# Kernel optimization log

Measured on AMD Instinct MI355X. Metric: run time of the kernel, lower is better.

## Reference

```python
import jax, jax.numpy as jnp
import numpy as np


def _window_indices(L, K):
    # 0-based (emo, cau) index pairs kept in the torch flattening order:
    # emo varies slowly (outer), cau varies fast (inner), |cau-emo| <= K.
    i = np.repeat(np.arange(L), L)
    j = np.tile(np.arange(L), L)
    m = np.abs(j - i) <= K
    return i[m], j[m]


def setup_inputs() -> dict:
    key = jax.random.key(0)
    ks = jax.random.split(key, 6)
    B, L, D = 4, 512, 768
    K, P = 10, 50
    R = 2 * D + P  # rank_feat_dim = 1586
    return {
        "doc_sents_h": jax.random.normal(ks[0], (B, L, D), jnp.float32),
        "pos_emb": jax.random.normal(ks[1], (2 * K + 1, P), jnp.float32) * 0.05,
        "W1": jax.random.normal(ks[2], (R, R), jnp.float32) * (1.0 / np.sqrt(R)),
        "b1": jax.random.normal(ks[3], (R,), jnp.float32) * 0.01,
        "W2": jax.random.normal(ks[4], (R, 1), jnp.float32) * (1.0 / np.sqrt(R)),
        "b2": jax.random.normal(ks[5], (1,), jnp.float32) * 0.01,
    }


def reference(doc_sents_h, pos_emb, W1, b1, W2, b2):
    B, L, D = doc_sents_h.shape
    K = (pos_emb.shape[0] - 1) // 2
    ei, ci = _window_indices(L, K)           # static numpy, shape [n]
    rel = jnp.asarray(ci - ei)               # [n] in [-K, K]
    # windowed pair features, [B, n, 2D] (skips the O(L^2) materialization)
    P_pairs = jnp.concatenate([doc_sents_h[:, ei], doc_sents_h[:, ci]], axis=-1)
    emb = pos_emb[rel + K]                   # [n, pos_dim]
    relf = rel.astype(pos_emb.dtype)
    kernel = jnp.exp(-jnp.square(relf[:, None] - relf[None, :]))  # [n, n]
    emb = kernel @ emb                       # [n, pos_dim], batch-invariant
    couples = jnp.concatenate(
        [P_pairs, jnp.broadcast_to(emb, (B,) + emb.shape)], axis=-1)  # [B, n, R]
    h = jax.nn.relu(couples @ W1 + b1)       # [B, n, R]
    pred = (h @ W2 + b2)[..., 0]             # [B, n]
    emo_cau_pos = jnp.stack(
        [jnp.asarray(ei) + 1, jnp.asarray(ci) + 1], axis=1)  # [n, 2], 1-based
    return pred, emo_cau_pos, h
```

## Files before the change

kernel.cpp:

```cpp
#include <hip/hip_runtime.h>
#include <math.h>

#define B_   4
#define L_   512
#define D_   768
#define K_   10
#define P_   50
#define R_   1586
#define NP_  10642
#define MROWS 2048
#define NPAD 1664
#define UVS  1600

#define PRED_OFF 0
#define POS_OFF  (B_ * NP_)
#define H_OFF    (B_ * NP_ + NP_ * 2)

typedef __attribute__((ext_vector_type(8))) short short8;
typedef __attribute__((ext_vector_type(4))) float floatx4;

__device__ __forceinline__ unsigned short f2bf(float f) {
    union { float f; unsigned int u; } a; a.f = f;
    unsigned int u = a.u;
    return (unsigned short)((u + 0x7FFF + ((u >> 16) & 1)) >> 16);
}
__device__ __forceinline__ float bf2f(unsigned short u) {
    union { unsigned int u; float f; } a; a.u = ((unsigned int)u) << 16;
    return a.f;
}

__device__ __forceinline__ int pair_offset(int i) {
    int h = i < K_ ? i : K_;
    int off = h * (K_ + 1) + (h * (h - 1)) / 2;
    if (i > K_) {
        int fullEnd = i < (L_ - K_) ? i : (L_ - K_);
        off += (fullEnd - K_) * (2 * K_ + 1);
        if (i > L_ - K_) {
            int t = i - (L_ - K_);
            int first = 2 * K_;
            int last = L_ + K_ - (i - 1);
            off += (first + last) * t / 2;
        }
    }
    return off;
}

__global__ __launch_bounds__(256) void convert_A(
        const float* __restrict__ doc, unsigned short* __restrict__ At) {
    int idx = (blockIdx.x * 256 + threadIdx.x) * 4;
    float4 v = *(const float4*)(doc + idx);
    ushort4 o;
    o.x = f2bf(v.x); o.y = f2bf(v.y); o.z = f2bf(v.z); o.w = f2bf(v.w);
    *(ushort4*)(At + idx) = o;
}

__global__ __launch_bounds__(256) void convert_W(
        const float* __restrict__ W1, unsigned short* __restrict__ Wt) {
    int z = blockIdx.z;
    int k0 = blockIdx.x * 32;
    int n0 = blockIdx.y * 32;
    __shared__ float tile[32][33];
    int tx = threadIdx.x & 31, ty = threadIdx.x >> 5;
    #pragma unroll
    for (int r = 0; r < 4; ++r) {
        int k = k0 + ty + r * 8;
        int n = n0 + tx;
        tile[ty + r * 8][tx] = (n < R_) ? W1[(size_t)(z * D_ + k) * R_ + n] : 0.f;
    }
    __syncthreads();
    #pragma unroll
    for (int r = 0; r < 4; ++r) {
        int n = n0 + ty + r * 8;
        int k = k0 + tx;
        Wt[(size_t)z * NPAD * D_ + (size_t)n * D_ + k] = f2bf(tile[tx][ty + r * 8]);
    }
}

__global__ __launch_bounds__(256) void build_F(
        const float* __restrict__ pos_emb, const float* __restrict__ W1,
        const float* __restrict__ b1, unsigned short* __restrict__ Fb) {
    int s = blockIdx.x;
    __shared__ float Es[P_];
    if (threadIdx.x < P_) {
        float acc = 0.f;
        #pragma unroll
        for (int r = 0; r <= 2 * K_; ++r) {
            float cnt = (float)(L_ - (r > K_ ? r - K_ : K_ - r));
            float d = (float)(s - r);
            acc += cnt * expf(-d * d) * pos_emb[r * P_ + threadIdx.x];
        }
        Es[threadIdx.x] = acc;
    }
    __syncthreads();
    for (int j = threadIdx.x; j < R_; j += blockDim.x) {
        float acc = b1[j];
        #pragma unroll 10
        for (int p = 0; p < P_; ++p)
            acc += Es[p] * W1[(2 * D_ + p) * R_ + j];
        Fb[s * UVS + j] = f2bf(acc);
    }
}

#define GLOAD_LDS16(g, l) __builtin_amdgcn_global_load_lds( \
    (const __attribute__((address_space(1))) void*)(g), \
    (__attribute__((address_space(3))) void*)(l), 16, 0, 0)

__global__ __launch_bounds__(256) void gemm_mfma(
        const unsigned short* __restrict__ At,
        const unsigned short* __restrict__ Wt,
        unsigned short* __restrict__ U, unsigned short* __restrict__ V) {
    __shared__ unsigned short Alds[128 * 32];
    __shared__ unsigned short Blds[128 * 32];
    const int tileN = blockIdx.x * 128;
    const int tileM = blockIdx.y * 128;
    const unsigned short* Bt = Wt + (size_t)blockIdx.z * NPAD * D_;
    unsigned short* C = blockIdx.z ? V : U;

    const int lane = threadIdx.x & 63;
    const int w = threadIdx.x >> 6;
    const int wm = (w & 1) * 64, wn = (w >> 1) * 64;
    const int quad = lane >> 4, l16 = lane & 15;

    floatx4 acc[4][4] = {};

    for (int k0 = 0; k0 < D_; k0 += 32) {
        #pragma unroll
        for (int t = 0; t < 2; ++t) {
            int g = (t * 4 + w) * 64 + lane;
            int m = g >> 2, c = g & 3;
            GLOAD_LDS16(At + (size_t)(tileM + m) * D_ + k0 + c * 8,
                        Alds + (t * 4 + w) * 512);
            GLOAD_LDS16(Bt + (size_t)(tileN + m) * D_ + k0 + c * 8,
                        Blds + (t * 4 + w) * 512);
        }
        __syncthreads();
        short8 a[4], b[4];
        #pragma unroll
        for (int im = 0; im < 4; ++im)
            a[im] = *(const short8*)&Alds[(wm + im * 16 + l16) * 32 + quad * 8];
        #pragma unroll
        for (int in = 0; in < 4; ++in)
            b[in] = *(const short8*)&Blds[(wn + in * 16 + l16) * 32 + quad * 8];
        #pragma unroll
        for (int im = 0; im < 4; ++im)
            #pragma unroll
            for (int in = 0; in < 4; ++in)
                acc[im][in] = __builtin_amdgcn_mfma_f32_16x16x32_bf16(
                    a[im], b[in], acc[im][in], 0, 0, 0);
        __syncthreads();
    }
    #pragma unroll
    for (int im = 0; im < 4; ++im) {
        #pragma unroll
        for (int in = 0; in < 4; ++in) {
            int col = tileN + wn + in * 16 + l16;
            if (col < R_) {
                #pragma unroll
                for (int r = 0; r < 4; ++r) {
                    int row = tileM + wm + im * 16 + quad * 4 + r;
                    C[(size_t)row * UVS + col] = f2bf(acc[im][in][r]);
                }
            }
        }
    }
}

#define NC2 13
__global__ __launch_bounds__(256) void epilogue(
        const unsigned short* __restrict__ U, const unsigned short* __restrict__ V,
        const unsigned short* __restrict__ Fb, const float* __restrict__ W2,
        const float* __restrict__ b2, float* __restrict__ out) {
    const int w    = threadIdx.x >> 6;
    const int lane = threadIdx.x & 63;
    const int i    = blockIdx.x * 4 + w;
    const int b    = blockIdx.y;
    const int half = blockIdx.z;

    const ushort2* u2  = (const ushort2*)(U + (size_t)(b * L_ + i) * UVS);
    const float2*  w2v = (const float2*)W2;

    float2 ur[NC2], wr[NC2];
    #pragma unroll
    for (int t = 0; t < NC2; ++t) {
        int c = lane + t * 64;
        if (c < R_ / 2) {
            ushort2 uu = u2[c];
            ur[t] = make_float2(bf2f(uu.x), bf2f(uu.y));
            wr[t] = w2v[c];
        }
    }

    const int base = i - K_ > 0 ? i - K_ : 0;
    const int poff = pair_offset(i);
    const float bias = b2[0];
    const int dj0 = half ? 11 : 0;
    const int dj1 = half ? 21 : 11;

    for (int dj = dj0; dj < dj1; ++dj) {
        int j = i - K_ + dj;
        if (j < 0 || j >= L_) continue;
        int p = poff + (j - base);
        const ushort2* v2 = (const ushort2*)(V + (size_t)(b * L_ + j) * UVS);
        const ushort2* f2 = (const ushort2*)(Fb + (size_t)dj * UVS);
        double* h2 = (double*)(out + H_OFF + (size_t)(b * NP_ + p) * R_);

        float acc = 0.f;
        #pragma unroll
        for (int t = 0; t < NC2; ++t) {
            int c = lane + t * 64;
            if (c < R_ / 2) {
                ushort2 vv = v2[c], ff = f2[c];
                float h0 = fmaxf(ur[t].x + bf2f(vv.x) + bf2f(ff.x), 0.f);
                float h1 = fmaxf(ur[t].y + bf2f(vv.y) + bf2f(ff.y), 0.f);
                union { float2 f; double d; } pk;
                pk.f = make_float2(h0, h1);
                __builtin_nontemporal_store(pk.d, h2 + c);
                acc += h0 * wr[t].x + h1 * wr[t].y;
            }
        }
        #pragma unroll
        for (int off = 32; off; off >>= 1) acc += __shfl_down(acc, off, 64);
        if (lane == 0) {
            out[PRED_OFF + b * NP_ + p] = acc + bias;
            if (b == 0) {
                out[POS_OFF + p * 2 + 0] = (float)(i + 1);
                out[POS_OFF + p * 2 + 1] = (float)(j + 1);
            }
        }
    }
}

extern "C" void kernel_launch(void* const* d_in, const int* in_sizes, int n_in,
                              void* d_out, int out_size, void* d_ws, size_t ws_size,
                              hipStream_t stream) {
    const float* doc     = (const float*)d_in[0];
    const float* pos_emb = (const float*)d_in[1];
    const float* W1      = (const float*)d_in[2];
    const float* b1      = (const float*)d_in[3];
    const float* W2      = (const float*)d_in[4];
    const float* b2      = (const float*)d_in[5];
    float* out = (float*)d_out;

    char* ws = (char*)d_ws;
    size_t off = 0;
    unsigned short* U  = (unsigned short*)(ws + off); off += (size_t)MROWS * UVS * 2;
    unsigned short* V  = (unsigned short*)(ws + off); off += (size_t)MROWS * UVS * 2;
    unsigned short* Fb = (unsigned short*)(ws + off); off += (size_t)21 * UVS * 2;
    off = (off + 255) & ~(size_t)255;
    unsigned short* At = (unsigned short*)(ws + off); off += (size_t)MROWS * D_ * 2;
    off = (off + 255) & ~(size_t)255;
    unsigned short* Wt = (unsigned short*)(ws + off);

    convert_A<<<MROWS * D_ / 1024, 256, 0, stream>>>(doc, At);
    convert_W<<<dim3(D_ / 32, NPAD / 32, 2), 256, 0, stream>>>(W1, Wt);
    build_F<<<21, 256, 0, stream>>>(pos_emb, W1, b1, Fb);
    gemm_mfma<<<dim3(NPAD / 128, MROWS / 128, 2), 256, 0, stream>>>(At, Wt, U, V);
    epilogue<<<dim3(L_ / 4, B_, 2), 256, 0, stream>>>(U, V, Fb, W2, b2, out);
}
```

Measured before the change: 372.7 us.

## Merge prep kernels into one launch and remap epilogue to one row per block

Combines the bf16 conversion of A, the transposed conversion of W1 and the positional-feature build into a single kernel, with block ranges choosing the task. This removes two launches and their gaps. The epilogue now gives each block one (batch, row) pair, and its four waves stride over the 21 window offsets. U and W2 are therefore loaded once per row rather than once per half. The catch is fewer, wider blocks with uneven wave work near the sequence edges, plus branch divergence across blocks inside the fused prep kernel.

```diff
diff --git a/kernel.cpp b/kernel.cpp
--- a/kernel.cpp
+++ b/kernel.cpp
@@ -45,42 +45,47 @@
     return off;
 }
 
-__global__ __launch_bounds__(256) void convert_A(
-        const float* __restrict__ doc, unsigned short* __restrict__ At) {
-    int idx = (blockIdx.x * 256 + threadIdx.x) * 4;
-    float4 v = *(const float4*)(doc + idx);
-    ushort4 o;
-    o.x = f2bf(v.x); o.y = f2bf(v.y); o.z = f2bf(v.z); o.w = f2bf(v.w);
-    *(ushort4*)(At + idx) = o;
-}
-
-__global__ __launch_bounds__(256) void convert_W(
-        const float* __restrict__ W1, unsigned short* __restrict__ Wt) {
-    int z = blockIdx.z;
-    int k0 = blockIdx.x * 32;
-    int n0 = blockIdx.y * 32;
+#define CA_BLOCKS 1536
+#define CW_BLOCKS 2496
+__global__ __launch_bounds__(256) void prep(
+        const float* __restrict__ doc, const float* __restrict__ pos_emb,
+        const float* __restrict__ W1, const float* __restrict__ b1,
+        unsigned short* __restrict__ At, unsigned short* __restrict__ Wt,
+        unsigned short* __restrict__ Fb) {
     __shared__ float tile[32][33];
-    int tx = threadIdx.x & 31, ty = threadIdx.x >> 5;
-    #pragma unroll
-    for (int r = 0; r < 4; ++r) {
-        int k = k0 + ty + r * 8;
-        int n = n0 + tx;
-        tile[ty + r * 8][tx] = (n < R_) ? W1[(size_t)(z * D_ + k) * R_ + n] : 0.f;
-    }
-    __syncthreads();
-    #pragma unroll
-    for (int r = 0; r < 4; ++r) {
-        int n = n0 + ty + r * 8;
-        int k = k0 + tx;
-        Wt[(size_t)z * NPAD * D_ + (size_t)n * D_ + k] = f2bf(tile[tx][ty + r * 8]);
-    }
-}
-
-__global__ __launch_bounds__(256) void build_F(
-        const float* __restrict__ pos_emb, const float* __restrict__ W1,
-        const float* __restrict__ b1, unsigned short* __restrict__ Fb) {
-    int s = blockIdx.x;
     __shared__ float Es[P_];
+    const int bid = blockIdx.x;
+
+    if (bid < CA_BLOCKS) {
+        int idx = (bid * 256 + threadIdx.x) * 4;
+        float4 v = *(const float4*)(doc + idx);
+        ushort4 o;
+        o.x = f2bf(v.x); o.y = f2bf(v.y); o.z = f2bf(v.z); o.w = f2bf(v.w);
+        *(ushort4*)(At + idx) = o;
+        return;
+    }
+    if (bid < CA_BLOCKS + CW_BLOCKS) {
+        int bb = bid - CA_BLOCKS;
+        int z = bb / 1248, rem = bb % 1248;
+        int k0 = (rem % 24) * 32;
+        int n0 = (rem / 24) * 32;
+        int tx = threadIdx.x & 31, ty = threadIdx.x >> 5;
+        #pragma unroll
+        for (int r = 0; r < 4; ++r) {
+            int k = k0 + ty + r * 8;
+            int n = n0 + tx;
+            tile[ty + r * 8][tx] = (n < R_) ? W1[(size_t)(z * D_ + k) * R_ + n] : 0.f;
+        }
+        __syncthreads();
+        #pragma unroll
+        for (int r = 0; r < 4; ++r) {
+            int n = n0 + ty + r * 8;
+            int k = k0 + tx;
+            Wt[(size_t)z * NPAD * D_ + (size_t)n * D_ + k] = f2bf(tile[tx][ty + r * 8]);
+        }
+        return;
+    }
+    int s = bid - (CA_BLOCKS + CW_BLOCKS);
     if (threadIdx.x < P_) {
         float acc = 0.f;
         #pragma unroll
@@ -92,7 +97,7 @@
         Es[threadIdx.x] = acc;
     }
     __syncthreads();
-    for (int j = threadIdx.x; j < R_; j += blockDim.x) {
+    for (int j = threadIdx.x; j < R_; j += 256) {
         float acc = b1[j];
         #pragma unroll 10
         for (int p = 0; p < P_; ++p)
@@ -172,9 +177,8 @@
         const float* __restrict__ b2, float* __restrict__ out) {
     const int w    = threadIdx.x >> 6;
     const int lane = threadIdx.x & 63;
-    const int i    = blockIdx.x * 4 + w;
-    const int b    = blockIdx.y;
-    const int half = blockIdx.z;
+    const int b    = blockIdx.x >> 9;
+    const int i    = blockIdx.x & (L_ - 1);
 
     const ushort2* u2  = (const ushort2*)(U + (size_t)(b * L_ + i) * UVS);
     const float2*  w2v = (const float2*)W2;
@@ -193,12 +197,10 @@
     const int base = i - K_ > 0 ? i - K_ : 0;
     const int poff = pair_offset(i);
     const float bias = b2[0];
-    const int dj0 = half ? 11 : 0;
-    const int dj1 = half ? 21 : 11;
-
-    for (int dj = dj0; dj < dj1; ++dj) {
+
+    for (int dj = w; dj < 2 * K_ + 1; dj += 4) {
         int j = i - K_ + dj;
-        if (j < 0 || j >= L_) continue;
+        if ((unsigned)j >= L_) continue;
         int p = poff + (j - base);
         const ushort2* v2 = (const ushort2*)(V + (size_t)(b * L_ + j) * UVS);
         const ushort2* f2 = (const ushort2*)(Fb + (size_t)dj * UVS);
@@ -251,9 +253,8 @@
     off = (off + 255) & ~(size_t)255;
     unsigned short* Wt = (unsigned short*)(ws + off);
 
-    convert_A<<<MROWS * D_ / 1024, 256, 0, stream>>>(doc, At);
-    convert_W<<<dim3(D_ / 32, NPAD / 32, 2), 256, 0, stream>>>(W1, Wt);
-    build_F<<<21, 256, 0, stream>>>(pos_emb, W1, b1, Fb);
+    prep<<<CA_BLOCKS + CW_BLOCKS + 21, 256, 0, stream>>>(
+        doc, pos_emb, W1, b1, At, Wt, Fb);
     gemm_mfma<<<dim3(NPAD / 128, MROWS / 128, 2), 256, 0, stream>>>(At, Wt, U, V);
-    epilogue<<<dim3(L_ / 4, B_, 2), 256, 0, stream>>>(U, V, Fb, W2, b2, out);
-}
+    epilogue<<<dim3(MROWS), 256, 0, stream>>>(U, V, Fb, W2, b2, out);
+}
```

Result: faster. 361.1 us (-3.1%).
